# Optimization experiments

Measured on AMD Instinct MI355X. Metric: run time of the kernel, lower is better.

Reference implementation:

```python
import jax, jax.numpy as jnp
import numpy as np

NUM_HEADS = 32
NUM_KV_HEADS = 8
HEAD_DIM = 128


def setup_inputs() -> dict:
    key = jax.random.key(0)
    ks = jax.random.split(key, 5)
    B, S, H = 2, 2048, 4096
    Dq = NUM_HEADS * HEAD_DIM      # 4096
    Dkv = NUM_KV_HEADS * HEAD_DIM  # 1024
    return {
        "hidden_states": jax.random.normal(ks[0], (B, S, H), jnp.float32),
        "w_q": jax.random.normal(ks[1], (H, Dq), jnp.float32) * 0.02,
        "w_k": jax.random.normal(ks[2], (H, Dkv), jnp.float32) * 0.02,
        "w_v": jax.random.normal(ks[3], (H, Dkv), jnp.float32) * 0.02,
        "w_o": jax.random.normal(ks[4], (Dq, H), jnp.float32) * 0.02,
    }


def reference(hidden_states, w_q, w_k, w_v, w_o):
    # GQA causal attention, prefill path (no KV cache, RoPE is a no-op in source).
    B, S, _ = hidden_states.shape
    Hq, Hkv, D = NUM_HEADS, NUM_KV_HEADS, HEAD_DIM
    g = Hq // Hkv  # kv groups
    scale = D ** -0.5

    q = (hidden_states @ w_q).reshape(B, S, Hkv, g, D)  # [B,S,Hkv,g,D]
    k = (hidden_states @ w_k).reshape(B, S, Hkv, D)     # [B,S,Hkv,D]
    v = (hidden_states @ w_v).reshape(B, S, Hkv, D)

    # repeat_kv expressed as grouped einsum (avoids materializing repeated K/V)
    scores = jnp.einsum('bqhgd,bkhd->bhgqk', q, k) * scale  # [B,Hkv,g,S,S]
    causal = jnp.tril(jnp.ones((S, S), dtype=bool))
    scores = jnp.where(causal, scores, -jnp.inf)
    probs = jax.nn.softmax(scores.astype(jnp.float32), axis=-1).astype(q.dtype)

    attn = jnp.einsum('bhgqk,bkhd->bqhgd', probs, v)  # [B,S,Hkv,g,D]
    attn = attn.reshape(B, S, Hq * D)
    return attn @ w_o
```

## Files before the change

kernel.cpp:

```cpp
#include <hip/hip_runtime.h>

typedef unsigned short u16;
typedef __attribute__((ext_vector_type(8))) short bf16x8;
typedef __attribute__((ext_vector_type(8))) unsigned short u16x8;
typedef __attribute__((ext_vector_type(4))) unsigned short u16x4;
typedef __attribute__((ext_vector_type(4))) float f32x4;

__device__ __forceinline__ u16 f2bf(float f) {
  union { float f; unsigned u; } v; v.f = f;
  unsigned r = v.u + 0x7fffu + ((v.u >> 16) & 1u);
  return (u16)(r >> 16);
}

__device__ __forceinline__ void gload16(const u16* g, u16* l) {
  __builtin_amdgcn_global_load_lds((const __attribute__((address_space(1))) void*)g,
                                   (__attribute__((address_space(3))) void*)l, 16, 0, 0);
}

__global__ __launch_bounds__(256) void cast_bf16_kern(const float* __restrict__ in,
                                                      u16* __restrict__ out, int n) {
  int i = (blockIdx.x * 256 + threadIdx.x) * 8;
  if (i >= n) return;
  float4 a = *(const float4*)(in + i);
  float4 b = *(const float4*)(in + i + 4);
  u16x8 r;
  r[0] = f2bf(a.x); r[1] = f2bf(a.y); r[2] = f2bf(a.z); r[3] = f2bf(a.w);
  r[4] = f2bf(b.x); r[5] = f2bf(b.y); r[6] = f2bf(b.z); r[7] = f2bf(b.w);
  *(u16x8*)(out + i) = r;
}

__global__ __launch_bounds__(256) void transpose_cast_kern(const float* __restrict__ in,
                                                           u16* __restrict__ out, int K, int N) {
  __shared__ float tile[64][65];
  int nbx = N >> 6;
  int n0 = (blockIdx.x % nbx) << 6;
  int k0 = (blockIdx.x / nbx) << 6;
  int tx = threadIdx.x & 15;
  int ty = threadIdx.x >> 4;
#pragma unroll
  for (int r = 0; r < 64; r += 16) {
    float4 v = *(const float4*)(in + (size_t)(k0 + ty + r) * N + n0 + tx * 4);
    tile[ty + r][tx * 4 + 0] = v.x;
    tile[ty + r][tx * 4 + 1] = v.y;
    tile[ty + r][tx * 4 + 2] = v.z;
    tile[ty + r][tx * 4 + 3] = v.w;
  }
  __syncthreads();
#pragma unroll
  for (int r = 0; r < 64; r += 16) {
    u16x4 o;
#pragma unroll
    for (int j = 0; j < 4; j++) o[j] = f2bf(tile[tx * 4 + j][ty + r]);
    *(u16x4*)(out + (size_t)(n0 + ty + r) * K + k0 + tx * 4) = o;
  }
}

template <int MODE>
__global__ __launch_bounds__(256) void gemm_bt(const u16* __restrict__ A,
                                               const u16* __restrict__ Bt,
                                               void* __restrict__ Cout,
                                               void* __restrict__ Cout2,
                                               int M, int N, int K) {
  __shared__ u16 As[128 * 32];
  __shared__ u16 Bs[128 * 32];
  const int tid = threadIdx.x;
  const int lane = tid & 63, wv = tid >> 6;
  const int wr = wv >> 1, wc = wv & 1;
  const int li = lane & 15, lg = lane >> 4;
  const int nbx = N >> 7;
  const int m0 = (blockIdx.x / nbx) << 7;
  const int n0 = (blockIdx.x % nbx) << 7;

  f32x4 acc[4][4];
#pragma unroll
  for (int m = 0; m < 4; m++)
#pragma unroll
    for (int n = 0; n < 4; n++) acc[m][n] = (f32x4){0.f, 0.f, 0.f, 0.f};

  const int srow = wv * 16 + (lane >> 2);
  const int skoff = (lane & 3) * 8;
  const u16* ag0 = A + (size_t)(m0 + srow) * K + skoff;
  const u16* ag1 = A + (size_t)(m0 + srow + 64) * K + skoff;
  const u16* bg0 = Bt + (size_t)(n0 + srow) * K + skoff;
  const u16* bg1 = Bt + (size_t)(n0 + srow + 64) * K + skoff;
  u16* al = As + wv * 512;
  u16* bl = Bs + wv * 512;

  for (int kt = 0; kt < K; kt += 32) {
    __syncthreads();
    gload16(ag0 + kt, al);
    gload16(ag1 + kt, al + 2048);
    gload16(bg0 + kt, bl);
    gload16(bg1 + kt, bl + 2048);
    __syncthreads();
    bf16x8 af[4], bfr[4];
#pragma unroll
    for (int m = 0; m < 4; m++)
      af[m] = *(const bf16x8*)(As + (wr * 64 + m * 16 + li) * 32 + lg * 8);
#pragma unroll
    for (int n = 0; n < 4; n++)
      bfr[n] = *(const bf16x8*)(Bs + (wc * 64 + n * 16 + li) * 32 + lg * 8);
#pragma unroll
    for (int m = 0; m < 4; m++)
#pragma unroll
      for (int n = 0; n < 4; n++)
        acc[m][n] = __builtin_amdgcn_mfma_f32_16x16x32_bf16(af[m], bfr[n], acc[m][n], 0, 0, 0);
  }

#pragma unroll
  for (int m = 0; m < 4; m++)
#pragma unroll
    for (int n = 0; n < 4; n++)
#pragma unroll
      for (int r = 0; r < 4; r++) {
        int gm = m0 + wr * 64 + m * 16 + lg * 4 + r;
        int gn = n0 + wc * 64 + n * 16 + li;
        float val = acc[m][n][r];
        if (MODE == 0) {
          ((u16*)Cout)[(size_t)gm * N + gn] = f2bf(val);
        } else {
          if (gn < 1024) {
            ((u16*)Cout)[(size_t)gm * 1024 + gn] = f2bf(val);
          } else {
            int c = gn - 1024;
            int b = gm >> 11, s = gm & 2047, kvh = c >> 7, d = c & 127;
            ((u16*)Cout2)[(size_t)((b * 8 + kvh) * 128 + d) * 2048 + s] = f2bf(val);
          }
        }
      }
}

#define PH_PRE()                                           \
  asm volatile("" ::: "memory");                           \
  __builtin_amdgcn_s_barrier();                            \
  asm volatile("s_waitcnt lgkmcnt(0)" ::: "memory");       \
  __builtin_amdgcn_sched_barrier(0);                       \
  __builtin_amdgcn_s_setprio(1)

#define PH_POST()                                          \
  __builtin_amdgcn_s_setprio(0);                           \
  __builtin_amdgcn_sched_barrier(0);                       \
  asm volatile("" ::: "memory");                           \
  __builtin_amdgcn_s_barrier()

template <int MODE>
__global__ __launch_bounds__(512, 2) void gemm256(const u16* __restrict__ A,
                                                  const u16* __restrict__ Bt,
                                                  void* __restrict__ Cout,
                                                  int M, int N, int K) {
  __shared__ u16 lds[65536];
  const int tid = threadIdx.x;
  const int lane = tid & 63, w = tid >> 6;
  const int wm = w >> 2, wn = w & 3;
  const int li = lane & 15, lg = lane >> 4;
  const int NT = K >> 6;

  const int nbx = N >> 8;
  const int nwg = gridDim.x;
  const int swz = (blockIdx.x & 7) * (nwg >> 3) + (blockIdx.x >> 3);
  const int m0 = (swz / nbx) << 8;
  const int n0 = (swz % nbx) << 8;

  const int srow = w * 16 + (lane >> 3);
  const int scol = ((lane & 7) ^ (lane >> 3)) << 3;
  const u16* sA0 = A + (size_t)(m0 + srow) * K + scol;
  const u16* sA1 = A + (size_t)(m0 + 128 + srow) * K + scol;
  const u16* sB0 = Bt + (size_t)(n0 + srow) * K + scol;
  const u16* sB1 = Bt + (size_t)(n0 + 128 + srow) * K + scol;
  const size_t jK = (size_t)8 * K;
  u16* dA0 = lds + w * 1024;
  u16* dA1 = lds + 8192 + w * 1024;
  u16* dB0 = lds + 32768 + w * 1024;
  u16* dB1 = lds + 32768 + 8192 + w * 1024;

#define STG(sp, dp, t_) do {                                          \
    int db_ = (t_) & 1;                                               \
    gload16((sp) + (size_t)(t_) * 64, (dp) + db_ * 16384);            \
    gload16((sp) + (size_t)(t_) * 64 + jK, (dp) + db_ * 16384 + 512); \
  } while (0)

  STG(sA0, dA0, 0); STG(sA1, dA1, 0); STG(sB0, dB0, 0); STG(sB1, dB1, 0);
  STG(sA0, dA0, 1); STG(sA1, dA1, 1); STG(sB0, dB0, 1); STG(sB1, dB1, 1);
  asm volatile("s_waitcnt vmcnt(8)" ::: "memory");
  asm volatile("" ::: "memory");
  __builtin_amdgcn_s_barrier();

  f32x4 acc[8][4];
#pragma unroll
  for (int m = 0; m < 8; m++)
#pragma unroll
    for (int n = 0; n < 4; n++) acc[m][n] = (f32x4){0.f, 0.f, 0.f, 0.f};

  const int xsw = (li & 7) << 3;
  const int k0o = (lg * 8) ^ xsw;
  const int k1o = (32 + lg * 8) ^ xsw;
  const u16* aBase = lds + wm * 8192;
  const u16* bBase = lds + 32768 + (wn >> 1) * 8192;
  const int brow0 = (wn & 1) * 64;

  bf16x8 a[4][2], b[4][2];

  for (int t = 0; t < NT; ++t) {
    const int db = t & 1;
    const u16* Ab = aBase + db * 16384;
    const u16* Bb = bBase + db * 16384;

#pragma unroll
    for (int mf = 0; mf < 4; mf++) {
      int r = mf * 16 + li;
      a[mf][0] = *(const bf16x8*)(Ab + r * 64 + k0o);
      a[mf][1] = *(const bf16x8*)(Ab + r * 64 + k1o);
    }
#pragma unroll
    for (int nf = 0; nf < 2; nf++) {
      int r = brow0 + nf * 16 + li;
      b[nf][0] = *(const bf16x8*)(Bb + r * 64 + k0o);
      b[nf][1] = *(const bf16x8*)(Bb + r * 64 + k1o);
    }
    asm volatile("s_waitcnt lgkmcnt(8)" ::: "memory");
    PH_PRE();
#pragma unroll
    for (int mf = 0; mf < 4; mf++)
#pragma unroll
      for (int nf = 0; nf < 2; nf++) {
        acc[mf][nf] = __builtin_amdgcn_mfma_f32_16x16x32_bf16(a[mf][0], b[nf][0], acc[mf][nf], 0, 0, 0);
        acc[mf][nf] = __builtin_amdgcn_mfma_f32_16x16x32_bf16(a[mf][1], b[nf][1], acc[mf][nf], 0, 0, 0);
      }
    PH_POST();

#pragma unroll
    for (int nf = 2; nf < 4; nf++) {
      int r = brow0 + nf * 16 + li;
      b[nf][0] = *(const bf16x8*)(Bb + r * 64 + k0o);
      b[nf][1] = *(const bf16x8*)(Bb + r * 64 + k1o);
    }
    PH_PRE();
#pragma unroll
    for (int mf = 0; mf < 4; mf++)
#pragma unroll
      for (int nf = 2; nf < 4; nf++) {
        acc[mf][nf] = __builtin_amdgcn_mfma_f32_16x16x32_bf16(a[mf][0], b[nf][0], acc[mf][nf], 0, 0, 0);
        acc[mf][nf] = __builtin_amdgcn_mfma_f32_16x16x32_bf16(a[mf][1], b[nf][1], acc[mf][nf], 0, 0, 0);
      }
    PH_POST();

#pragma unroll
    for (int mf = 0; mf < 4; mf++) {
      int r = (mf + 4) * 16 + li;
      a[mf][0] = *(const bf16x8*)(Ab + r * 64 + k0o);
      a[mf][1] = *(const bf16x8*)(Ab + r * 64 + k1o);
    }
    if (t + 2 < NT) { STG(sB0, dB0, t + 2); STG(sB1, dB1, t + 2); }
    asm volatile("s_waitcnt lgkmcnt(4)" ::: "memory");
    PH_PRE();
#pragma unroll
    for (int mf = 0; mf < 4; mf++)
#pragma unroll
      for (int nf = 2; nf < 4; nf++) {
        acc[mf + 4][nf] = __builtin_amdgcn_mfma_f32_16x16x32_bf16(a[mf][0], b[nf][0], acc[mf + 4][nf], 0, 0, 0);
        acc[mf + 4][nf] = __builtin_amdgcn_mfma_f32_16x16x32_bf16(a[mf][1], b[nf][1], acc[mf + 4][nf], 0, 0, 0);
      }
    PH_POST();

    if (t + 2 < NT) { STG(sA0, dA0, t + 2); STG(sA1, dA1, t + 2); }
    PH_PRE();
#pragma unroll
    for (int mf = 0; mf < 4; mf++)
#pragma unroll
      for (int nf = 0; nf < 2; nf++) {
        acc[mf + 4][nf] = __builtin_amdgcn_mfma_f32_16x16x32_bf16(a[mf][0], b[nf][0], acc[mf + 4][nf], 0, 0, 0);
        acc[mf + 4][nf] = __builtin_amdgcn_mfma_f32_16x16x32_bf16(a[mf][1], b[nf][1], acc[mf + 4][nf], 0, 0, 0);
      }
    __builtin_amdgcn_s_setprio(0);
    __builtin_amdgcn_sched_barrier(0);
    if (t < NT - 2) {
      asm volatile("s_waitcnt vmcnt(8)" ::: "memory");
    } else {
      asm volatile("s_waitcnt vmcnt(0)" ::: "memory");
    }
    asm volatile("" ::: "memory");
    __builtin_amdgcn_s_barrier();
  }

#pragma unroll
  for (int mf = 0; mf < 8; mf++)
#pragma unroll
    for (int nf = 0; nf < 4; nf++)
#pragma unroll
      for (int r = 0; r < 4; r++) {
        int gm = m0 + wm * 128 + mf * 16 + lg * 4 + r;
        int gn = n0 + wn * 64 + nf * 16 + li;
        if (MODE == 0)
          ((u16*)Cout)[(size_t)gm * N + gn] = f2bf(acc[mf][nf][r]);
        else
          ((float*)Cout)[(size_t)gm * N + gn] = acc[mf][nf][r];
      }
#undef STG
}

__global__ __launch_bounds__(256, 2) void flash_attn_kern(const u16* __restrict__ Qg,
                                                          const u16* __restrict__ Kg,
                                                          const u16* __restrict__ VT,
                                                          u16* __restrict__ Og) {
  const int bid = blockIdx.x;
  const int qt = 63 - (bid >> 4);
  const int gh = bid & 15;
  const int b = gh >> 3, kvh = gh & 7;
  const int tid = threadIdx.x;
  const int lane = tid & 63, w = tid >> 6;
  const int li = lane & 15, lg = lane >> 4;
  const int h = kvh * 4 + w;
  const int q0 = qt << 5;
  const int nt = (qt >> 1) + 1;

  __shared__ u16 Kbuf[2][8192];
  __shared__ u16 Vbuf[2][8192];
  __shared__ u16 Ps[4][16 * 72];

  bf16x8 qf[2][4];
  {
    const u16* qp = Qg + ((size_t)(b * 2048 + q0 + li)) * 4096 + h * 128 + lg * 8;
#pragma unroll
    for (int m = 0; m < 2; m++)
#pragma unroll
      for (int ks = 0; ks < 4; ks++)
        qf[m][ks] = *(const bf16x8*)(qp + (size_t)(m * 16) * 4096 + ks * 32);
  }

  const u16* ksrc[4];
  const u16* vsrc[4];
#pragma unroll
  for (int i = 0; i < 4; i++) {
    int c = w * 4 + i;
    int krow = c * 4 + (lane >> 4);
    int kinner = ((lane & 15) * 16) ^ ((krow & 7) << 4);
    ksrc[i] = Kg + (size_t)(b * 2048 + krow) * 1024 + kvh * 128 + (kinner >> 1);
    int vrow = c * 8 + (lane >> 3);
    int vinner = ((lane & 7) * 16) ^ ((vrow & 7) << 4);
    vsrc[i] = VT + (size_t)((b * 8 + kvh) * 128 + vrow) * 2048 + (vinner >> 1);
  }
#pragma unroll
  for (int i = 0; i < 4; i++) {
    int c = w * 4 + i;
    gload16(ksrc[i], &Kbuf[0][c * 512]);
    gload16(vsrc[i], &Vbuf[0][c * 512]);
    ksrc[i] += 64 * 1024;
    vsrc[i] += 64;
  }

  f32x4 oa[2][8];
#pragma unroll
  for (int m = 0; m < 2; m++)
#pragma unroll
    for (int n = 0; n < 8; n++) oa[m][n] = (f32x4){0.f, 0.f, 0.f, 0.f};
  f32x4 lacc[2];
  lacc[0] = (f32x4){0.f, 0.f, 0.f, 0.f};
  lacc[1] = (f32x4){0.f, 0.f, 0.f, 0.f};
  float mrun[2][4];
#pragma unroll
  for (int m = 0; m < 2; m++)
#pragma unroll
    for (int r = 0; r < 4; r++) mrun[m][r] = -1e30f;

  const float scale = 0.08838834764831845f;
  bf16x8 onesf;
#pragma unroll
  for (int j = 0; j < 8; j++) onesf[j] = (short)0x3F80;

  asm volatile("s_waitcnt vmcnt(0)\n\ts_barrier" ::: "memory");

  for (int t = 0; t < nt; ++t) {
    const int cur = t & 1;
    const u16* KB = Kbuf[cur];
    const u16* VB = Vbuf[cur];
    if (t + 1 < nt) {
#pragma unroll
      for (int i = 0; i < 4; i++) {
        int c = w * 4 + i;
        gload16(ksrc[i], &Kbuf[cur ^ 1][c * 512]);
        gload16(vsrc[i], &Vbuf[cur ^ 1][c * 512]);
        ksrc[i] += 64 * 1024;
        vsrc[i] += 64;
      }
    }

    f32x4 sacc[2][4];
#pragma unroll
    for (int m = 0; m < 2; m++)
#pragma unroll
      for (int n = 0; n < 4; n++) sacc[m][n] = (f32x4){0.f, 0.f, 0.f, 0.f};
    __builtin_amdgcn_s_setprio(1);
#pragma unroll
    for (int n = 0; n < 4; n++) {
      int krow = n * 16 + li;
      const u16* kb = KB + krow * 128;
      int sw = (krow & 7) << 4;
#pragma unroll
      for (int ks = 0; ks < 4; ks++) {
        bf16x8 kf = *(const bf16x8*)(kb + (((ks * 64 + lg * 16) ^ sw) >> 1));
        sacc[0][n] = __builtin_amdgcn_mfma_f32_16x16x32_bf16(qf[0][ks], kf, sacc[0][n], 0, 0, 0);
        sacc[1][n] = __builtin_amdgcn_mfma_f32_16x16x32_bf16(qf[1][ks], kf, sacc[1][n], 0, 0, 0);
      }
    }
    __builtin_amdgcn_s_setprio(0);

#pragma unroll
    for (int m = 0; m < 2; m++)
#pragma unroll
      for (int n = 0; n < 4; n++)
#pragma unroll
        for (int r = 0; r < 4; r++) sacc[m][n][r] *= scale;
    if (t == nt - 1) {
      const int kv0 = t * 64;
#pragma unroll
      for (int m = 0; m < 2; m++)
#pragma unroll
        for (int r = 0; r < 4; r++) {
          int q = q0 + m * 16 + lg * 4 + r;
#pragma unroll
          for (int n = 0; n < 4; n++)
            if (kv0 + n * 16 + li > q) sacc[m][n][r] = -1e30f;
        }
    }

#pragma unroll
    for (int m = 0; m < 2; m++)
#pragma unroll
      for (int r = 0; r < 4; r++) {
        float mx = fmaxf(fmaxf(sacc[m][0][r], sacc[m][1][r]), fmaxf(sacc[m][2][r], sacc[m][3][r]));
        mx = fmaxf(mx, __shfl_xor(mx, 1, 64));
        mx = fmaxf(mx, __shfl_xor(mx, 2, 64));
        mx = fmaxf(mx, __shfl_xor(mx, 4, 64));
        mx = fmaxf(mx, __shfl_xor(mx, 8, 64));
        float mnew = fmaxf(mrun[m][r], mx);
        float corr = __expf(mrun[m][r] - mnew);
        mrun[m][r] = mnew;
#pragma unroll
        for (int n = 0; n < 4; n++) sacc[m][n][r] = __expf(sacc[m][n][r] - mnew);
        lacc[m][r] *= corr;
#pragma unroll
        for (int n = 0; n < 8; n++) oa[m][n][r] *= corr;
      }

    bf16x8 pf[2][2];
    u16* Pw = Ps[w];
#pragma unroll
    for (int m = 0; m < 2; m++) {
#pragma unroll
      for (int n = 0; n < 4; n++)
#pragma unroll
        for (int r = 0; r < 4; r++)
          Pw[(lg * 4 + r) * 72 + n * 16 + li] = f2bf(sacc[m][n][r]);
      asm volatile("s_waitcnt lgkmcnt(0)" ::: "memory");
#pragma unroll
      for (int kvs = 0; kvs < 2; kvs++)
        pf[m][kvs] = *(const bf16x8*)(Pw + li * 72 + kvs * 32 + lg * 8);
      asm volatile("s_waitcnt lgkmcnt(0)" ::: "memory");
      __builtin_amdgcn_sched_barrier(0);
    }

    __builtin_amdgcn_s_setprio(1);
#pragma unroll
    for (int kvs = 0; kvs < 2; kvs++) {
#pragma unroll
      for (int n = 0; n < 8; n++) {
        int vrow = n * 16 + li;
        bf16x8 vf = *(const bf16x8*)(VB + vrow * 64 +
                                     (((kvs * 64 + lg * 16) ^ ((vrow & 7) << 4)) >> 1));
        oa[0][n] = __builtin_amdgcn_mfma_f32_16x16x32_bf16(pf[0][kvs], vf, oa[0][n], 0, 0, 0);
        oa[1][n] = __builtin_amdgcn_mfma_f32_16x16x32_bf16(pf[1][kvs], vf, oa[1][n], 0, 0, 0);
      }
      lacc[0] = __builtin_amdgcn_mfma_f32_16x16x32_bf16(pf[0][kvs], onesf, lacc[0], 0, 0, 0);
      lacc[1] = __builtin_amdgcn_mfma_f32_16x16x32_bf16(pf[1][kvs], onesf, lacc[1], 0, 0, 0);
    }
    __builtin_amdgcn_s_setprio(0);

    asm volatile("s_waitcnt vmcnt(0)\n\ts_barrier" ::: "memory");
  }

#pragma unroll
  for (int m = 0; m < 2; m++) {
    float inv[4];
#pragma unroll
    for (int r = 0; r < 4; r++) inv[r] = 1.0f / lacc[m][r];
    u16* op = Og + (size_t)(b * 2048 + q0 + m * 16 + lg * 4) * 4096 + h * 128 + li;
#pragma unroll
    for (int r = 0; r < 4; r++)
#pragma unroll
      for (int n = 0; n < 8; n++)
        op[(size_t)r * 4096 + n * 16] = f2bf(oa[m][n][r] * inv[r]);
  }
}

extern "C" void kernel_launch(void* const* d_in, const int* in_sizes, int n_in,
                              void* d_out, int out_size, void* d_ws, size_t ws_size,
                              hipStream_t stream) {
  (void)in_sizes; (void)n_in; (void)out_size; (void)ws_size;
  const float* hs = (const float*)d_in[0];
  const float* wq = (const float*)d_in[1];
  const float* wk = (const float*)d_in[2];
  const float* wv = (const float*)d_in[3];
  const float* wo = (const float*)d_in[4];

  u16* ws   = (u16*)d_ws;
  u16* hs_b = ws;
  u16* wqT  = hs_b + 16777216;
  u16* wkT  = wqT + 16777216;
  u16* wvT  = wkT + 4194304;
  u16* woT  = wvT + 4194304;
  u16* Qb   = woT + 16777216;
  u16* Kb   = Qb + 16777216;
  u16* VTb  = Kb + 4194304;
  u16* attnb = VTb + 4194304;

  cast_bf16_kern<<<8192, 256, 0, stream>>>(hs, hs_b, 16777216);
  transpose_cast_kern<<<4096, 256, 0, stream>>>(wq, wqT, 4096, 4096);
  transpose_cast_kern<<<1024, 256, 0, stream>>>(wk, wkT, 4096, 1024);
  transpose_cast_kern<<<1024, 256, 0, stream>>>(wv, wvT, 4096, 1024);
  transpose_cast_kern<<<4096, 256, 0, stream>>>(wo, woT, 4096, 4096);

  gemm256<0><<<256, 512, 0, stream>>>(hs_b, wqT, Qb, 4096, 4096, 4096);
  gemm_bt<3><<<512, 256, 0, stream>>>(hs_b, wkT, Kb, VTb, 4096, 2048, 4096);

  flash_attn_kern<<<1024, 256, 0, stream>>>(Qb, Kb, VTb, attnb);

  gemm256<2><<<256, 512, 0, stream>>>(attnb, woT, (float*)d_out, 4096, 4096, 4096);
}
```

Measured before the change: 541.3 us.

## Compute transposed S in flash attention to keep P in registers

After: 517.0 us. 4.5% less time.

```diff
diff --git a/kernel.cpp b/kernel.cpp
--- a/kernel.cpp
+++ b/kernel.cpp
@@ -124,7 +124,8 @@
           } else {
             int c = gn - 1024;
             int b = gm >> 11, s = gm & 2047, kvh = c >> 7, d = c & 127;
-            ((u16*)Cout2)[(size_t)((b * 8 + kvh) * 128 + d) * 2048 + s] = f2bf(val);
+            int s2 = (s & ~31) | (((s >> 2) & 3) << 3) | (((s >> 4) & 1) << 2) | (s & 3);
+            ((u16*)Cout2)[(size_t)((b * 8 + kvh) * 128 + d) * 2048 + s2] = f2bf(val);
           }
         }
       }
@@ -315,7 +316,6 @@
 
   __shared__ u16 Kbuf[2][8192];
   __shared__ u16 Vbuf[2][8192];
-  __shared__ u16 Ps[4][16 * 72];
 
   bf16x8 qf[2][4];
   {
@@ -356,11 +356,7 @@
   f32x4 lacc[2];
   lacc[0] = (f32x4){0.f, 0.f, 0.f, 0.f};
   lacc[1] = (f32x4){0.f, 0.f, 0.f, 0.f};
-  float mrun[2][4];
-#pragma unroll
-  for (int m = 0; m < 2; m++)
-#pragma unroll
-    for (int r = 0; r < 4; r++) mrun[m][r] = -1e30f;
+  float mrun[2] = {-1e30f, -1e30f};
 
   const float scale = 0.08838834764831845f;
   bf16x8 onesf;
@@ -398,8 +394,8 @@
 #pragma unroll
       for (int ks = 0; ks < 4; ks++) {
         bf16x8 kf = *(const bf16x8*)(kb + (((ks * 64 + lg * 16) ^ sw) >> 1));
-        sacc[0][n] = __builtin_amdgcn_mfma_f32_16x16x32_bf16(qf[0][ks], kf, sacc[0][n], 0, 0, 0);
-        sacc[1][n] = __builtin_amdgcn_mfma_f32_16x16x32_bf16(qf[1][ks], kf, sacc[1][n], 0, 0, 0);
+        sacc[0][n] = __builtin_amdgcn_mfma_f32_16x16x32_bf16(kf, qf[0][ks], sacc[0][n], 0, 0, 0);
+        sacc[1][n] = __builtin_amdgcn_mfma_f32_16x16x32_bf16(kf, qf[1][ks], sacc[1][n], 0, 0, 0);
       }
     }
     __builtin_amdgcn_s_setprio(0);
@@ -413,51 +409,50 @@
     if (t == nt - 1) {
       const int kv0 = t * 64;
 #pragma unroll
-      for (int m = 0; m < 2; m++)
-#pragma unroll
-        for (int r = 0; r < 4; r++) {
-          int q = q0 + m * 16 + lg * 4 + r;
-#pragma unroll
-          for (int n = 0; n < 4; n++)
-            if (kv0 + n * 16 + li > q) sacc[m][n][r] = -1e30f;
-        }
-    }
-
+      for (int m = 0; m < 2; m++) {
+        int q = q0 + m * 16 + li;
+#pragma unroll
+        for (int n = 0; n < 4; n++)
+#pragma unroll
+          for (int r = 0; r < 4; r++)
+            if (kv0 + n * 16 + lg * 4 + r > q) sacc[m][n][r] = -1e30f;
+      }
+    }
+
+#pragma unroll
+    for (int m = 0; m < 2; m++) {
+      float mx = sacc[m][0][0];
+#pragma unroll
+      for (int n = 0; n < 4; n++)
+#pragma unroll
+        for (int r = 0; r < 4; r++) mx = fmaxf(mx, sacc[m][n][r]);
+      mx = fmaxf(mx, __shfl_xor(mx, 16, 64));
+      mx = fmaxf(mx, __shfl_xor(mx, 32, 64));
+      float mnew = fmaxf(mrun[m], mx);
+      float corr = __expf(mrun[m] - mnew);
+      mrun[m] = mnew;
+#pragma unroll
+      for (int n = 0; n < 4; n++)
+#pragma unroll
+        for (int r = 0; r < 4; r++) sacc[m][n][r] = __expf(sacc[m][n][r] - mnew);
+#pragma unroll
+      for (int r = 0; r < 4; r++) lacc[m][r] *= corr;
+#pragma unroll
+      for (int n = 0; n < 8; n++)
+#pragma unroll
+        for (int r = 0; r < 4; r++) oa[m][n][r] *= corr;
+    }
+
+    bf16x8 pf[2][2];
 #pragma unroll
     for (int m = 0; m < 2; m++)
 #pragma unroll
-      for (int r = 0; r < 4; r++) {
-        float mx = fmaxf(fmaxf(sacc[m][0][r], sacc[m][1][r]), fmaxf(sacc[m][2][r], sacc[m][3][r]));
-        mx = fmaxf(mx, __shfl_xor(mx, 1, 64));
-        mx = fmaxf(mx, __shfl_xor(mx, 2, 64));
-        mx = fmaxf(mx, __shfl_xor(mx, 4, 64));
-        mx = fmaxf(mx, __shfl_xor(mx, 8, 64));
-        float mnew = fmaxf(mrun[m][r], mx);
-        float corr = __expf(mrun[m][r] - mnew);
-        mrun[m][r] = mnew;
-#pragma unroll
-        for (int n = 0; n < 4; n++) sacc[m][n][r] = __expf(sacc[m][n][r] - mnew);
-        lacc[m][r] *= corr;
-#pragma unroll
-        for (int n = 0; n < 8; n++) oa[m][n][r] *= corr;
-      }
-
-    bf16x8 pf[2][2];
-    u16* Pw = Ps[w];
-#pragma unroll
-    for (int m = 0; m < 2; m++) {
-#pragma unroll
-      for (int n = 0; n < 4; n++)
-#pragma unroll
-        for (int r = 0; r < 4; r++)
-          Pw[(lg * 4 + r) * 72 + n * 16 + li] = f2bf(sacc[m][n][r]);
-      asm volatile("s_waitcnt lgkmcnt(0)" ::: "memory");
-#pragma unroll
-      for (int kvs = 0; kvs < 2; kvs++)
-        pf[m][kvs] = *(const bf16x8*)(Pw + li * 72 + kvs * 32 + lg * 8);
-      asm volatile("s_waitcnt lgkmcnt(0)" ::: "memory");
-      __builtin_amdgcn_sched_barrier(0);
-    }
+      for (int kvs = 0; kvs < 2; kvs++) {
+        u16x8 pw;
+#pragma unroll
+        for (int e = 0; e < 8; e++) pw[e] = f2bf(sacc[m][2 * kvs + (e >> 2)][e & 3]);
+        pf[m][kvs] = *(bf16x8*)&pw;
+      }
 
     __builtin_amdgcn_s_setprio(1);
 #pragma unroll
@@ -467,11 +462,11 @@
         int vrow = n * 16 + li;
         bf16x8 vf = *(const bf16x8*)(VB + vrow * 64 +
                                      (((kvs * 64 + lg * 16) ^ ((vrow & 7) << 4)) >> 1));
-        oa[0][n] = __builtin_amdgcn_mfma_f32_16x16x32_bf16(pf[0][kvs], vf, oa[0][n], 0, 0, 0);
-        oa[1][n] = __builtin_amdgcn_mfma_f32_16x16x32_bf16(pf[1][kvs], vf, oa[1][n], 0, 0, 0);
-      }
-      lacc[0] = __builtin_amdgcn_mfma_f32_16x16x32_bf16(pf[0][kvs], onesf, lacc[0], 0, 0, 0);
-      lacc[1] = __builtin_amdgcn_mfma_f32_16x16x32_bf16(pf[1][kvs], onesf, lacc[1], 0, 0, 0);
+        oa[0][n] = __builtin_amdgcn_mfma_f32_16x16x32_bf16(vf, pf[0][kvs], oa[0][n], 0, 0, 0);
+        oa[1][n] = __builtin_amdgcn_mfma_f32_16x16x32_bf16(vf, pf[1][kvs], oa[1][n], 0, 0, 0);
+      }
+      lacc[0] = __builtin_amdgcn_mfma_f32_16x16x32_bf16(onesf, pf[0][kvs], lacc[0], 0, 0, 0);
+      lacc[1] = __builtin_amdgcn_mfma_f32_16x16x32_bf16(onesf, pf[1][kvs], lacc[1], 0, 0, 0);
     }
     __builtin_amdgcn_s_setprio(0);
 
@@ -480,15 +475,15 @@
 
 #pragma unroll
   for (int m = 0; m < 2; m++) {
-    float inv[4];
-#pragma unroll
-    for (int r = 0; r < 4; r++) inv[r] = 1.0f / lacc[m][r];
-    u16* op = Og + (size_t)(b * 2048 + q0 + m * 16 + lg * 4) * 4096 + h * 128 + li;
-#pragma unroll
-    for (int r = 0; r < 4; r++)
-#pragma unroll
-      for (int n = 0; n < 8; n++)
-        op[(size_t)r * 4096 + n * 16] = f2bf(oa[m][n][r] * inv[r]);
+    float inv = 1.0f / lacc[m][0];
+    u16* op = Og + (size_t)(b * 2048 + q0 + m * 16 + li) * 4096 + h * 128 + lg * 4;
+#pragma unroll
+    for (int n = 0; n < 8; n++) {
+      u16x4 o;
+#pragma unroll
+      for (int r = 0; r < 4; r++) o[r] = f2bf(oa[m][n][r] * inv);
+      *(u16x4*)(op + n * 16) = o;
+    }
   }
 }
 
```
